# Kernel optimization log

Measured on AMD Instinct MI355X. Metric: run time of the kernel, lower is better.

## Reference

```python
import jax, jax.numpy as jnp
import numpy as np

B, T, L, F = 32, 512, 16, 128   # utterances, max frames, frame-spec width, specgram_height
H = 128                          # hidden_size1 == hidden_size2
C = 61                           # TIMIT phoneme count


def _p(key, shape, scale):
    return jax.random.normal(key, shape, jnp.float32) * scale


def setup_inputs() -> dict:
    key = jax.random.key(0)
    ks = jax.random.split(key, 32)
    s = 1.0 / np.sqrt(H)
    inp = {}
    inp["x"] = jax.random.normal(ks[0], (B, T, L, F), jnp.float32)
    inp["lengths"] = jax.random.randint(ks[1], (B,), T // 2, T + 1, jnp.int32)
    i = 2
    # rnn1: tanh-RNN, 2 layers, bidirectional (layer0 in=F, layer1 in=2H); dir axis 0
    for name, din in (("r1l0", F), ("r1l1", 2 * H)):
        inp[name + "_Wih"] = _p(ks[i], (2, H, din), s); i += 1
        inp[name + "_Whh"] = _p(ks[i], (2, H, H), s); i += 1
        inp[name + "_bih"] = _p(ks[i], (2, H), s); i += 1
        inp[name + "_bhh"] = _p(ks[i], (2, H), s); i += 1
    # rnn2: GRU, 2 layers, bidirectional (in=2H for both layers); gates packed r,z,n
    for name in ("g0", "g1"):
        inp[name + "_Wih"] = _p(ks[i], (2, 3 * H, 2 * H), s); i += 1
        inp[name + "_Whh"] = _p(ks[i], (2, 3 * H, H), s); i += 1
        inp[name + "_bih"] = _p(ks[i], (2, 3 * H), s); i += 1
        inp[name + "_bhh"] = _p(ks[i], (2, 3 * H), s); i += 1
    inp["fc_W"] = _p(ks[i], (C, 2 * H), s); i += 1
    inp["fc_b"] = _p(ks[i], (C,), s)
    return inp


def _rnn_bidir(x, Wih, Whh, bih, bhh):
    # x: (N, S, din) -> (N, S, 2H); PyTorch nn.RNN(tanh), bidirectional
    outs = []
    for d in range(2):
        xw = jnp.einsum('bli,hi->blh', x, Wih[d]) + bih[d]
        W, b = Whh[d], bhh[d]
        def step(h, xt):
            h = jnp.tanh(xt + h @ W.T + b)
            return h, h
        h0 = jnp.zeros((x.shape[0], W.shape[0]), x.dtype)
        _, ys = jax.lax.scan(step, h0, jnp.swapaxes(xw, 0, 1), reverse=(d == 1))
        outs.append(jnp.swapaxes(ys, 0, 1))
    return jnp.concatenate(outs, -1)


def _gru_bidir(x, Wih, Whh, bih, bhh):
    # x: (N, S, din) -> (N, S, 2H); PyTorch nn.GRU, bidirectional
    outs = []
    for d in range(2):
        xw = jnp.einsum('bli,hi->blh', x, Wih[d]) + bih[d]  # (N, S, 3H)
        W, b = Whh[d], bhh[d]
        def step(h, xt):
            g = h @ W.T + b
            xr, xz, xn = jnp.split(xt, 3, -1)
            gr, gz, gn = jnp.split(g, 3, -1)
            r = jax.nn.sigmoid(xr + gr)
            z = jax.nn.sigmoid(xz + gz)
            n = jnp.tanh(xn + r * gn)
            h = (1.0 - z) * n + z * h
            return h, h
        h0 = jnp.zeros((x.shape[0], W.shape[1]), x.dtype)
        _, ys = jax.lax.scan(step, h0, jnp.swapaxes(xw, 0, 1), reverse=(d == 1))
        outs.append(jnp.swapaxes(ys, 0, 1))
    return jnp.concatenate(outs, -1)


def reference(x, lengths,
              r1l0_Wih, r1l0_Whh, r1l0_bih, r1l0_bhh,
              r1l1_Wih, r1l1_Whh, r1l1_bih, r1l1_bhh,
              g0_Wih, g0_Whh, g0_bih, g0_bhh,
              g1_Wih, g1_Whh, g1_bih, g1_bhh,
              fc_W, fc_b):
    b, t, l, f = x.shape
    # per-sample rnn1 loop == one batched pass over all B*T frames (eval mode: no dropout)
    o = _rnn_bidir(x.reshape(b * t, l, f), r1l0_Wih, r1l0_Whh, r1l0_bih, r1l0_bhh)
    o = _rnn_bidir(o, r1l1_Wih, r1l1_Whh, r1l1_bih, r1l1_bhh)
    o = o[:, -1, :].reshape(b, t, 2 * H)       # last inner timestep per frame
    o = _gru_bidir(o, g0_Wih, g0_Whh, g0_bih, g0_bhh)
    o = _gru_bidir(o, g1_Wih, g1_Whh, g1_bih, g1_bhh)
    logits = o @ fc_W.T + fc_b                  # (B, T, C)
    mask = jnp.arange(t)[None, :] < lengths[:, None]
    # ragged scatter: concat first lengths[i] timesteps of each sample
    return logits.reshape(b * t, -1)[mask.reshape(-1)]
```

## Files before the change

### kernel.cpp

```cpp
#include <hip/hip_runtime.h>
#include <hip/hip_bf16.h>

#define B_ 32
#define T_ 512
#define L_ 16
#define F_ 128
#define H_ 128
#define C_ 61
#define NF_ (B_*T_)
#define CH_ 4096

typedef unsigned int u32;
typedef unsigned short u16;
typedef __attribute__((ext_vector_type(8))) short s16x8;
typedef __attribute__((ext_vector_type(4))) float f32x4;

__device__ __forceinline__ float bflo(u32 v){ return __uint_as_float(v << 16); }
__device__ __forceinline__ float bfhi(u32 v){ return __uint_as_float(v & 0xffff0000u); }
__device__ __forceinline__ u16 f2bf(float f){
  u32 u = __float_as_uint(f);
  u += 0x7fffu + ((u >> 16) & 1u);
  return (u16)(u >> 16);
}
__device__ __forceinline__ u32 pack2(float a, float b){
  return (u32)f2bf(a) | ((u32)f2bf(b) << 16);
}
__device__ __forceinline__ float fast_tanh(float x){
  float e = __expf(2.f*x);
  return 1.f - 2.f*__builtin_amdgcn_rcpf(e + 1.f);
}
__device__ __forceinline__ float fast_sigmoid(float x){
  return __builtin_amdgcn_rcpf(1.f + __expf(-x));
}
__device__ __forceinline__ f32x4 mfma16(s16x8 a, s16x8 b, f32x4 c){
  return __builtin_amdgcn_mfma_f32_16x16x32_bf16(a, b, c, 0, 0, 0);
}
__device__ __forceinline__ s16x8 packfrag(const float* p){
  const float4 a = *(const float4*)p;
  const float4 b = *(const float4*)(p+4);
  union { s16x8 v; u32 w[4]; } f;
  f.w[0]=pack2(a.x,a.y); f.w[1]=pack2(a.z,a.w);
  f.w[2]=pack2(b.x,b.y); f.w[3]=pack2(b.z,b.w);
  return f.v;
}

__global__ __launch_bounds__(256) void l0_mfma(
    const float* __restrict__ x,
    const float* __restrict__ Wih,
    const float* __restrict__ Whh,
    const float* __restrict__ bih,
    const float* __restrict__ bhh,
    u16* __restrict__ out)
{
  __shared__ __align__(16) u16 Hb[2][32][136];
  __shared__ __align__(16) u16 Xb[2][32][136];
  const int t = threadIdx.x;
  const int lane = t & 63, wv = t >> 6;
  const int l15 = lane & 15, kg = lane >> 4;
  const int dir = blockIdx.y;
  const int f0 = blockIdx.x * 32;
  s16x8 wih[2][4], whh[2][4];
  {
    const float* Wid = Wih + dir*16384;
    const float* Whd = Whh + dir*16384;
    #pragma unroll
    for (int nt = 0; nt < 2; nt++){
      const int u = wv*32 + nt*16 + l15;
      #pragma unroll
      for (int kc = 0; kc < 4; kc++){
        const int k = kc*32 + kg*8;
        wih[nt][kc] = packfrag(&Wid[u*128 + k]);
        whh[nt][kc] = packfrag(&Whd[u*128 + k]);
      }
    }
  }
  float bv[2];
  bv[0] = bih[dir*128 + wv*32 + l15]      + bhh[dir*128 + wv*32 + l15];
  bv[1] = bih[dir*128 + wv*32 + 16 + l15] + bhh[dir*128 + wv*32 + 16 + l15];
  const int sr = t >> 3, sc = (t & 7) * 16;
  {
    *(uint4*)&Hb[0][sr][sc]   = make_uint4(0,0,0,0);
    *(uint4*)&Hb[0][sr][sc+8] = make_uint4(0,0,0,0);
    const int s0 = dir ? 15 : 0;
    const float4* xp = (const float4*)&x[(size_t)(f0+sr)*2048 + s0*128 + sc];
    const float4 v0 = xp[0], v1 = xp[1], v2 = xp[2], v3 = xp[3];
    *(uint4*)&Xb[0][sr][sc]   = make_uint4(pack2(v0.x,v0.y),pack2(v0.z,v0.w),
                                           pack2(v1.x,v1.y),pack2(v1.z,v1.w));
    *(uint4*)&Xb[0][sr][sc+8] = make_uint4(pack2(v2.x,v2.y),pack2(v2.z,v2.w),
                                           pack2(v3.x,v3.y),pack2(v3.z,v3.w));
  }
  __syncthreads();
  int cur = 0;
  for (int st = 0; st < 16; st++){
    const int s = dir ? (15-st) : st;
    float4 p0,p1,p2,p3;
    if (st < 15){
      const int sn = dir ? (14-st) : (st+1);
      const float4* xp = (const float4*)&x[(size_t)(f0+sr)*2048 + sn*128 + sc];
      p0 = xp[0]; p1 = xp[1]; p2 = xp[2]; p3 = xp[3];
    }
    f32x4 acc00 = {0.f,0.f,0.f,0.f}, acc01 = acc00, acc10 = acc00, acc11 = acc00;
    #pragma unroll
    for (int kc = 0; kc < 4; kc++){
      const int ko = kc*32 + kg*8;
      const s16x8 ax0 = *(const s16x8*)&Xb[cur][l15][ko];
      const s16x8 ax1 = *(const s16x8*)&Xb[cur][16+l15][ko];
      const s16x8 ah0 = *(const s16x8*)&Hb[cur][l15][ko];
      const s16x8 ah1 = *(const s16x8*)&Hb[cur][16+l15][ko];
      acc00 = mfma16(ax0, wih[0][kc], acc00);
      acc01 = mfma16(ax0, wih[1][kc], acc01);
      acc10 = mfma16(ax1, wih[0][kc], acc10);
      acc11 = mfma16(ax1, wih[1][kc], acc11);
      acc00 = mfma16(ah0, whh[0][kc], acc00);
      acc01 = mfma16(ah0, whh[1][kc], acc01);
      acc10 = mfma16(ah1, whh[0][kc], acc10);
      acc11 = mfma16(ah1, whh[1][kc], acc11);
    }
    const int u0 = wv*32 + l15, u1 = wv*32 + 16 + l15;
    u16* op = out + (size_t)f0*4096 + s*256 + dir*128;
    #pragma unroll
    for (int r = 0; r < 4; r++){
      const int m0r = kg*4 + r, m1r = 16 + kg*4 + r;
      u16 h00 = f2bf(fast_tanh(acc00[r] + bv[0]));
      u16 h01 = f2bf(fast_tanh(acc01[r] + bv[1]));
      u16 h10 = f2bf(fast_tanh(acc10[r] + bv[0]));
      u16 h11 = f2bf(fast_tanh(acc11[r] + bv[1]));
      Hb[cur^1][m0r][u0] = h00;
      Hb[cur^1][m0r][u1] = h01;
      Hb[cur^1][m1r][u0] = h10;
      Hb[cur^1][m1r][u1] = h11;
      op[(size_t)m0r*4096 + u0] = h00;
      op[(size_t)m0r*4096 + u1] = h01;
      op[(size_t)m1r*4096 + u0] = h10;
      op[(size_t)m1r*4096 + u1] = h11;
    }
    if (st < 15){
      *(uint4*)&Xb[cur^1][sr][sc]   = make_uint4(pack2(p0.x,p0.y),pack2(p0.z,p0.w),
                                                 pack2(p1.x,p1.y),pack2(p1.z,p1.w));
      *(uint4*)&Xb[cur^1][sr][sc+8] = make_uint4(pack2(p2.x,p2.y),pack2(p2.z,p2.w),
                                                 pack2(p3.x,p3.y),pack2(p3.z,p3.w));
    }
    __syncthreads();
    cur ^= 1;
  }
}

__global__ __launch_bounds__(256) void l1f_mfma(
    const u16* __restrict__ U,
    const float* __restrict__ Wih,
    const float* __restrict__ Whh,
    const float* __restrict__ bih,
    const float* __restrict__ bhh,
    u16* __restrict__ out)
{
  __shared__ __align__(16) u16 Hb[2][16][136];
  __shared__ __align__(16) u16 Xb[2][16][264];
  const int t = threadIdx.x;
  const int lane = t & 63, wv = t >> 6;
  const int l15 = lane & 15, kg = lane >> 4;
  const int f0 = blockIdx.x * 16;
  s16x8 wih[2][8], whh[2][4];
  {
    #pragma unroll
    for (int nt = 0; nt < 2; nt++){
      const int u = wv*32 + nt*16 + l15;
      #pragma unroll
      for (int kc = 0; kc < 8; kc++)
        wih[nt][kc] = packfrag(&Wih[u*256 + kc*32 + kg*8]);
      #pragma unroll
      for (int kc = 0; kc < 4; kc++)
        whh[nt][kc] = packfrag(&Whh[u*128 + kc*32 + kg*8]);
    }
  }
  float bv[2];
  bv[0] = bih[wv*32 + l15]      + bhh[wv*32 + l15];
  bv[1] = bih[wv*32 + 16 + l15] + bhh[wv*32 + 16 + l15];
  const int sr = t >> 4, scu = (t & 15) * 16;
  for (int idx = t; idx < 272; idx += 256)
    ((uint4*)&Hb[0][0][0])[idx] = make_uint4(0,0,0,0);
  {
    const uint4* up = (const uint4*)&U[(size_t)(f0+sr)*4096 + scu];
    uint4 c0 = up[0], c1 = up[1];
    *(uint4*)&Xb[0][sr][scu]   = c0;
    *(uint4*)&Xb[0][sr][scu+8] = c1;
  }
  __syncthreads();
  int cur = 0;
  for (int st = 0; st < 16; st++){
    uint4 c0,c1;
    if (st < 15){
      const uint4* up = (const uint4*)&U[(size_t)(f0+sr)*4096 + (st+1)*256 + scu];
      c0 = up[0]; c1 = up[1];
    }
    f32x4 acc0 = {0.f,0.f,0.f,0.f}, acc1 = acc0;
    #pragma unroll
    for (int kc = 0; kc < 8; kc++){
      const s16x8 ax = *(const s16x8*)&Xb[cur][l15][kc*32 + kg*8];
      acc0 = mfma16(ax, wih[0][kc], acc0);
      acc1 = mfma16(ax, wih[1][kc], acc1);
    }
    #pragma unroll
    for (int kc = 0; kc < 4; kc++){
      const s16x8 ah = *(const s16x8*)&Hb[cur][l15][kc*32 + kg*8];
      acc0 = mfma16(ah, whh[0][kc], acc0);
      acc1 = mfma16(ah, whh[1][kc], acc1);
    }
    const int u0 = wv*32 + l15, u1 = wv*32 + 16 + l15;
    #pragma unroll
    for (int r = 0; r < 4; r++){
      const int m = kg*4 + r;
      const u16 h0 = f2bf(fast_tanh(acc0[r] + bv[0]));
      const u16 h1 = f2bf(fast_tanh(acc1[r] + bv[1]));
      Hb[cur^1][m][u0] = h0;
      Hb[cur^1][m][u1] = h1;
      if (st == 15){
        out[(size_t)(f0+m)*256 + u0] = h0;
        out[(size_t)(f0+m)*256 + u1] = h1;
      }
    }
    if (st < 15){
      *(uint4*)&Xb[cur^1][sr][scu]   = c0;
      *(uint4*)&Xb[cur^1][sr][scu+8] = c1;
    }
    __syncthreads();
    cur ^= 1;
  }
}

__global__ __launch_bounds__(256) void mfma_gemm(
    const u16* __restrict__ A, int lda,
    const u16* __restrict__ Wb, int K,
    const float* __restrict__ bias,
    float* __restrict__ Cf, u16* __restrict__ Cb, int ldc, int act)
{
  const int t = threadIdx.x;
  const int lane = t & 63, wv = t >> 6;
  const int l15 = lane & 15, kg = lane >> 4;
  const int n0 = blockIdx.x * 32;
  const int m0 = blockIdx.y * 64 + wv*16;
  const u16* Ap = A + (size_t)(m0 + l15)*lda + kg*8;
  const u16* W0 = Wb + (size_t)(n0 + l15)*K + kg*8;
  const u16* W1 = Wb + (size_t)(n0 + 16 + l15)*K + kg*8;
  f32x4 acc0 = {0.f,0.f,0.f,0.f}, acc1 = acc0;
  #pragma unroll 4
  for (int kc = 0; kc < K/32; kc++){
    const s16x8 a  = *(const s16x8*)(Ap + kc*32);
    const s16x8 b0 = *(const s16x8*)(W0 + kc*32);
    const s16x8 b1 = *(const s16x8*)(W1 + kc*32);
    acc0 = mfma16(a, b0, acc0);
    acc1 = mfma16(a, b1, acc1);
  }
  const int col0 = n0 + l15, col1 = n0 + 16 + l15;
  const float bv0 = bias[col0], bv1 = bias[col1];
  #pragma unroll
  for (int r = 0; r < 4; r++){
    const int row = m0 + kg*4 + r;
    float v0 = acc0[r] + bv0, v1 = acc1[r] + bv1;
    if (act){ v0 = fast_tanh(v0); v1 = fast_tanh(v1); }
    if (Cf){
      Cf[(size_t)row*ldc + col0] = v0;
      Cf[(size_t)row*ldc + col1] = v1;
    } else {
      Cb[(size_t)row*ldc + col0] = f2bf(v0);
      Cb[(size_t)row*ldc + col1] = f2bf(v1);
    }
  }
}

__global__ __launch_bounds__(256) void gemm_xw(
    const u16* __restrict__ A, int lda,
    const u16* __restrict__ Wb, int K,
    const float* __restrict__ bias,
    float* __restrict__ xwT)
{
  const int t = threadIdx.x;
  const int lane = t & 63, wv = t >> 6;
  const int l15 = lane & 15, kg = lane >> 4;
  const int n0 = blockIdx.x * 32;
  const int m0 = blockIdx.y * 64 + wv*16;
  const u16* Ap = A + (size_t)(m0 + l15)*lda + kg*8;
  const u16* W0 = Wb + (size_t)(n0 + l15)*K + kg*8;
  const u16* W1 = Wb + (size_t)(n0 + 16 + l15)*K + kg*8;
  f32x4 acc0 = {0.f,0.f,0.f,0.f}, acc1 = acc0;
  #pragma unroll 4
  for (int kc = 0; kc < K/32; kc++){
    const s16x8 a  = *(const s16x8*)(Ap + kc*32);
    const s16x8 b0 = *(const s16x8*)(W0 + kc*32);
    const s16x8 b1 = *(const s16x8*)(W1 + kc*32);
    acc0 = mfma16(a, b0, acc0);
    acc1 = mfma16(a, b1, acc1);
  }
  const int col0 = n0 + l15, col1 = n0 + 16 + l15;
  const float bv0 = bias[col0], bv1 = bias[col1];
  const int row0 = m0 + kg*4;
  const int b   = row0 >> 9;
  const int tt0 = row0 & 511;
  const int half = b >> 4, kg2 = (b & 15) >> 2, r2 = b & 3;
  const int d0 = col0 >= 384, d1 = col1 >= 384;
  const int cc0 = col0 - d0*384, cc1 = col1 - d1*384;
  const size_t i0 = (((((size_t)d0*512 + tt0)*2 + half)*8 + (cc0>>7? 0:0) + ((cc0&127)>>4))*4 + kg2)*192
                    + (size_t)(cc0&15)*12 + (cc0>>7)*4 + r2;
  const size_t i1 = (((((size_t)d1*512 + tt0)*2 + half)*8 + ((cc1&127)>>4))*4 + kg2)*192
                    + (size_t)(cc1&15)*12 + (cc1>>7)*4 + r2;
  #pragma unroll
  for (int r = 0; r < 4; r++){
    xwT[i0 + (size_t)r*12288] = acc0[r] + bv0;
    xwT[i1 + (size_t)r*12288] = acc1[r] + bv1;
  }
}

__global__ __launch_bounds__(256) void prep_kernel(
    const float* __restrict__ g0W, const float* __restrict__ g1W,
    const float* __restrict__ r1Wih,
    const float* __restrict__ r1bih, const float* __restrict__ r1bhh,
    u16* __restrict__ g0o, u16* __restrict__ g1o, u16* __restrict__ r1o,
    float* __restrict__ bo)
{
  const int i = blockIdx.x*256 + threadIdx.x;
  if (i < 196608){ g0o[i] = f2bf(g0W[i]); g1o[i] = f2bf(g1W[i]); }
  if (i < 32768)   r1o[i] = f2bf(r1Wih[32768 + i]);
  if (i < 128)     bo[i]  = r1bih[128+i] + r1bhh[128+i];
}

__global__ __launch_bounds__(512) void gru_mfma(
    const float* __restrict__ xwT,
    const float* __restrict__ Whh,
    const float* __restrict__ bhh,
    u16* __restrict__ hout)
{
  __shared__ __align__(16) u16 h_lds[2][16][136];
  const int t = threadIdx.x;
  const int lane = t & 63, wv = t >> 6;
  const int l15 = lane & 15, kg = lane >> 4;
  const int dir = blockIdx.x & 1, half = blockIdx.x >> 1;
  const int b0 = half*16;
  const int us = wv*16;
  s16x8 wb[3][4];
  {
    const float* Wd = Whh + (size_t)dir*49152;
    #pragma unroll
    for (int g = 0; g < 3; g++)
      #pragma unroll
      for (int kc = 0; kc < 4; kc++)
        wb[g][kc] = packfrag(&Wd[(size_t)(g*128 + us + l15)*128 + kc*32 + kg*8]);
  }
  const float bh0 = bhh[dir*384 + us + l15];
  const float bh1 = bhh[dir*384 + 128 + us + l15];
  const float bh2 = bhh[dir*384 + 256 + us + l15];
  if (t < 272) ((uint4*)&h_lds[0][0][0])[t] = make_uint4(0,0,0,0);
  float hreg[4] = {0.f,0.f,0.f,0.f};
  const long tstep = dir ? -49152 : 49152;
  const char* xb = (const char*)xwT
      + ((size_t)dir*512 + (dir ? 511 : 0))*49152
      + (size_t)((((half*8 + wv)*4 + kg)*16 + l15)*12)*4;
  f32x4 px0[3], px1[3];
  px0[0] = *(const f32x4*)(xb); px0[1] = *(const f32x4*)(xb+16); px0[2] = *(const f32x4*)(xb+32);
  xb += tstep;
  px1[0] = *(const f32x4*)(xb); px1[1] = *(const f32x4*)(xb+16); px1[2] = *(const f32x4*)(xb+32);
  xb += tstep;
  const int hstep = dir ? -256 : 256;
  int hoff[4];
  #pragma unroll
  for (int r = 0; r < 4; r++)
    hoff[r] = ((b0 + kg*4 + r)*512 + (dir ? 511 : 0))*256 + dir*128 + us + l15;
  __syncthreads();
  int cur = 0;

#define GSTEP(PX)                                                           \
  {                                                                         \
    const s16x8 af0 = *(const s16x8*)&h_lds[cur][l15][kg*8];                \
    const s16x8 af1 = *(const s16x8*)&h_lds[cur][l15][32+kg*8];             \
    const s16x8 af2 = *(const s16x8*)&h_lds[cur][l15][64+kg*8];             \
    const s16x8 af3 = *(const s16x8*)&h_lds[cur][l15][96+kg*8];             \
    f32x4 a0 = {0.f,0.f,0.f,0.f}, a1 = a0, a2 = a0;                         \
    a0 = mfma16(af0, wb[0][0], a0);                                         \
    a1 = mfma16(af0, wb[1][0], a1);                                         \
    a2 = mfma16(af0, wb[2][0], a2);                                         \
    a0 = mfma16(af1, wb[0][1], a0);                                         \
    a1 = mfma16(af1, wb[1][1], a1);                                         \
    a2 = mfma16(af1, wb[2][1], a2);                                         \
    a0 = mfma16(af2, wb[0][2], a0);                                         \
    a1 = mfma16(af2, wb[1][2], a1);                                         \
    a2 = mfma16(af2, wb[2][2], a2);                                         \
    a0 = mfma16(af3, wb[0][3], a0);                                         \
    a1 = mfma16(af3, wb[1][3], a1);                                         \
    a2 = mfma16(af3, wb[2][3], a2);                                         \
    const f32x4 n0 = *(const f32x4*)(xb);                                   \
    const f32x4 n1 = *(const f32x4*)(xb+16);                                \
    const f32x4 n2 = *(const f32x4*)(xb+32);                                \
    xb += tstep;                                                            \
    _Pragma("unroll")                                                       \
    for (int r = 0; r < 4; r++){                                            \
      const float rr = fast_sigmoid(PX[0][r] + a0[r] + bh0);                \
      const float zz = fast_sigmoid(PX[1][r] + a1[r] + bh1);                \
      const float nn = fast_tanh(PX[2][r] + rr*(a2[r] + bh2));              \
      const float hn = fmaf(zz, hreg[r]-nn, nn);                            \
      hreg[r] = hn;                                                         \
      const u16 hb = f2bf(hn);                                              \
      h_lds[cur^1][kg*4+r][us+l15] = hb;                                    \
      hout[hoff[r]] = hb;                                                   \
      hoff[r] += hstep;                                                     \
    }                                                                       \
    PX[0] = n0; PX[1] = n1; PX[2] = n2;                                     \
    __syncthreads();                                                        \
    cur ^= 1;                                                               \
  }

  for (int ti = 0; ti < 512; ti += 2){
    GSTEP(px0);
    GSTEP(px1);
  }
#undef GSTEP
}

__global__ void prefix_kernel(const int* __restrict__ lengths, int* __restrict__ pre){
  if (threadIdx.x == 0 && blockIdx.x == 0){
    int run = 0;
    for (int b = 0; b < 32; b++){ pre[b] = run; run += lengths[b]; }
  }
}

__global__ __launch_bounds__(256) void fc_kernel(
    const u16* __restrict__ A,
    const float* __restrict__ W,
    const float* __restrict__ bias,
    const int* __restrict__ lengths,
    const int* __restrict__ pre,
    float* __restrict__ out)
{
  __shared__ __align__(16) float4 Wl[64][61];
  __shared__ __align__(16) float  Al[64][256];
  const int t = threadIdx.x;
  const int row0 = blockIdx.x * 64;
  for (int idx = t; idx < 61*64; idx += 256){
    int c = idx >> 6, k4 = idx & 63;
    Wl[k4][c] = *(const float4*)&W[(size_t)c*256 + k4*4];
  }
  {
    const u32* A32 = (const u32*)(A + (size_t)row0*256);
    for (int idx = t; idx < 8192; idx += 256){
      u32 v = A32[idx];
      int r = idx >> 7, kp = idx & 127;
      Al[r][2*kp]   = bflo(v);
      Al[r][2*kp+1] = bfhi(v);
    }
  }
  __syncthreads();
  const int c = t & 63;
  const int rbase = t >> 6;
  if (c < 61){
    const float bv = bias[c];
    for (int rr = rbase; rr < 64; rr += 4){
      float s0=0,s1=0,s2=0,s3=0;
      const float4* Ap = (const float4*)&Al[rr][0];
      #pragma unroll
      for (int k4 = 0; k4 < 64; k4++){
        const float4 w = Wl[k4][c];
        const float4 a = Ap[k4];
        s0 = fmaf(w.x, a.x, s0);
        s1 = fmaf(w.y, a.y, s1);
        s2 = fmaf(w.z, a.z, s2);
        s3 = fmaf(w.w, a.w, s3);
      }
      const int n = row0 + rr;
      const int b = n >> 9, tt = n & 511;
      if (tt < lengths[b])
        out[(size_t)(pre[b] + tt)*61 + c] = bv + s0+s1+s2+s3;
    }
  }
}

extern "C" void kernel_launch(void* const* d_in, const int* in_sizes, int n_in,
                              void* d_out, int out_size, void* d_ws, size_t ws_size,
                              hipStream_t stream)
{
  const float* x     = (const float*)d_in[0];
  const int*   lens  = (const int*)d_in[1];
  const float* r0Wih = (const float*)d_in[2];
  const float* r0Whh = (const float*)d_in[3];
  const float* r0bih = (const float*)d_in[4];
  const float* r0bhh = (const float*)d_in[5];
  const float* r1Wih = (const float*)d_in[6];
  const float* r1Whh = (const float*)d_in[7];
  const float* r1bih = (const float*)d_in[8];
  const float* r1bhh = (const float*)d_in[9];
  const float* g0Wih = (const float*)d_in[10];
  const float* g0Whh = (const float*)d_in[11];
  const float* g0bih = (const float*)d_in[12];
  const float* g0bhh = (const float*)d_in[13];
  const float* g1Wih = (const float*)d_in[14];
  const float* g1Whh = (const float*)d_in[15];
  const float* g1bih = (const float*)d_in[16];
  const float* g1bhh = (const float*)d_in[17];
  const float* fcW   = (const float*)d_in[18];
  const float* fcb   = (const float*)d_in[19];
  float* out = (float*)d_out;

  char* ws = (char*)d_ws;
  u16*   l0buf = (u16*)(ws);
  float* xwbuf = (float*)(ws);
  u16*   g0out = (u16*)(ws + 50331648);
  u16*   g0Wb  = (u16*)(ws + 58720256);
  u16*   g1Wb  = (u16*)(ws + 58720256 + 393216);
  u16*   r1Wb  = (u16*)(ws + 58720256 + 786432);
  float* biasb = (float*)(ws + 58720256 + 851968);
  u16*   g1out = (u16*)(ws + 58720256);
  u16*   rnn1  = (u16*)(ws + 67108864);
  int*   pre   = (int*)(ws + 75497472);

  prep_kernel<<<768, 256, 0, stream>>>(g0Wih, g1Wih, r1Wih, r1bih, r1bhh,
                                       g0Wb, g1Wb, r1Wb, biasb);
  for (int c = 0; c < NF_/CH_; c++){
    l0_mfma<<<dim3(CH_/32, 2), 256, 0, stream>>>(
        x + (size_t)c*CH_*2048, r0Wih, r0Whh, r0bih, r0bhh, l0buf);
    l1f_mfma<<<dim3(CH_/16), 256, 0, stream>>>(
        l0buf, r1Wih, r1Whh, r1bih, r1bhh, rnn1 + (size_t)c*CH_*256);
    mfma_gemm<<<dim3(128/32, CH_/64), 256, 0, stream>>>(
        l0buf + 15*256, 4096, r1Wb, 256, biasb,
        (float*)nullptr, rnn1 + (size_t)c*CH_*256 + 128, 256, 1);
  }
  gemm_xw<<<dim3(768/32, NF_/64), 256, 0, stream>>>(
      rnn1, 256, g0Wb, 256, g0bih, xwbuf);
  gru_mfma<<<4, 512, 0, stream>>>(xwbuf, g0Whh, g0bhh, g0out);
  gemm_xw<<<dim3(768/32, NF_/64), 256, 0, stream>>>(
      g0out, 256, g1Wb, 256, g1bih, xwbuf);
  gru_mfma<<<4, 512, 0, stream>>>(xwbuf, g1Whh, g1bhh, g1out);
  prefix_kernel<<<1, 64, 0, stream>>>(lens, pre);
  fc_kernel<<<NF_/64, 256, 0, stream>>>(g1out, fcW, fcb, lens, pre, out);
}
```

Measured before the change: 1.163 ms.

## Restructure GRU recurrence to 4 waves with transposed MFMA and folded r/z biases

The GRU recurrent kernel now runs 256 threads (4 waves) per block instead of 512, with each wave owning 32 hidden units across two 16-wide tiles. The MFMA operands are swapped so that each lane holds 4 consecutive hidden units, which lets h be written to LDS and global memory as packed uint2 stores. The xw precompute now folds the recurrent r and z biases into its output and writes a matching new layout. The intent is to cut per-step barrier cost and scalar store traffic on the serial critical path. In exchange each wave carries twice the weight registers and does twice the gate math per step, and the out-of-bounds prefetch on the final steps is dropped.

```diff
diff --git a/kernel.cpp b/kernel.cpp
--- a/kernel.cpp
+++ b/kernel.cpp
@@ -270,7 +270,7 @@
 __global__ __launch_bounds__(256) void gemm_xw(
     const u16* __restrict__ A, int lda,
     const u16* __restrict__ Wb, int K,
-    const float* __restrict__ bias,
+    const float* __restrict__ bih, const float* __restrict__ bhhp,
     float* __restrict__ xwT)
 {
   const int t = threadIdx.x;
@@ -291,17 +291,31 @@
     acc1 = mfma16(a, b1, acc1);
   }
   const int col0 = n0 + l15, col1 = n0 + 16 + l15;
-  const float bv0 = bias[col0], bv1 = bias[col1];
   const int row0 = m0 + kg*4;
-  const int b   = row0 >> 9;
-  const int tt0 = row0 & 511;
-  const int half = b >> 4, kg2 = (b & 15) >> 2, r2 = b & 3;
-  const int d0 = col0 >= 384, d1 = col1 >= 384;
-  const int cc0 = col0 - d0*384, cc1 = col1 - d1*384;
-  const size_t i0 = (((((size_t)d0*512 + tt0)*2 + half)*8 + (cc0>>7? 0:0) + ((cc0&127)>>4))*4 + kg2)*192
-                    + (size_t)(cc0&15)*12 + (cc0>>7)*4 + r2;
-  const size_t i1 = (((((size_t)d1*512 + tt0)*2 + half)*8 + ((cc1&127)>>4))*4 + kg2)*192
-                    + (size_t)(cc1&15)*12 + (cc1>>7)*4 + r2;
+  const int b = row0 >> 9, tt0 = row0 & 511;
+  const int half = b >> 4, bl = b & 15;
+  float bv0 = bih[col0], bv1 = bih[col1];
+  {
+    const int c0 = col0 >= 384 ? col0-384 : col0;
+    const int c1 = col1 >= 384 ? col1-384 : col1;
+    if ((c0 >> 7) < 2) bv0 += bhhp[col0];
+    if ((c1 >> 7) < 2) bv1 += bhhp[col1];
+  }
+  size_t i0, i1;
+  {
+    const int d0 = col0 >= 384 ? 1 : 0;
+    const int c  = col0 - d0*384;
+    const int g = c >> 7, cu = c & 127;
+    i0 = (((((size_t)d0*512 + tt0)*2 + half)*4 + (cu>>5))*4 + ((cu>>2)&3))*384
+         + (size_t)bl*24 + ((cu>>4)&1)*12 + g*4 + (cu&3);
+  }
+  {
+    const int d1 = col1 >= 384 ? 1 : 0;
+    const int c  = col1 - d1*384;
+    const int g = c >> 7, cu = c & 127;
+    i1 = (((((size_t)d1*512 + tt0)*2 + half)*4 + (cu>>5))*4 + ((cu>>2)&3))*384
+         + (size_t)bl*24 + ((cu>>4)&1)*12 + g*4 + (cu&3);
+  }
   #pragma unroll
   for (int r = 0; r < 4; r++){
     xwT[i0 + (size_t)r*12288] = acc0[r] + bv0;
@@ -322,7 +336,7 @@
   if (i < 128)     bo[i]  = r1bih[128+i] + r1bhh[128+i];
 }
 
-__global__ __launch_bounds__(512) void gru_mfma(
+__global__ __launch_bounds__(256, 1) void gru_mfma(
     const float* __restrict__ xwT,
     const float* __restrict__ Whh,
     const float* __restrict__ bhh,
@@ -333,83 +347,95 @@
   const int lane = t & 63, wv = t >> 6;
   const int l15 = lane & 15, kg = lane >> 4;
   const int dir = blockIdx.x & 1, half = blockIdx.x >> 1;
-  const int b0 = half*16;
-  const int us = wv*16;
-  s16x8 wb[3][4];
+  s16x8 wa[2][3][4];
   {
     const float* Wd = Whh + (size_t)dir*49152;
     #pragma unroll
-    for (int g = 0; g < 3; g++)
+    for (int t2 = 0; t2 < 2; t2++)
       #pragma unroll
-      for (int kc = 0; kc < 4; kc++)
-        wb[g][kc] = packfrag(&Wd[(size_t)(g*128 + us + l15)*128 + kc*32 + kg*8]);
-  }
-  const float bh0 = bhh[dir*384 + us + l15];
-  const float bh1 = bhh[dir*384 + 128 + us + l15];
-  const float bh2 = bhh[dir*384 + 256 + us + l15];
-  if (t < 272) ((uint4*)&h_lds[0][0][0])[t] = make_uint4(0,0,0,0);
-  float hreg[4] = {0.f,0.f,0.f,0.f};
-  const long tstep = dir ? -49152 : 49152;
+      for (int g = 0; g < 3; g++)
+        #pragma unroll
+        for (int kc = 0; kc < 4; kc++)
+          wa[t2][g][kc] = packfrag(&Wd[(size_t)(g*128 + wv*32 + t2*16 + l15)*128
+                                       + kc*32 + kg*8]);
+  }
+  f32x4 bhn[2];
+  bhn[0] = *(const f32x4*)&bhh[dir*384 + 256 + wv*32 + kg*4];
+  bhn[1] = *(const f32x4*)&bhh[dir*384 + 256 + wv*32 + 16 + kg*4];
+  {
+    const uint4 z = make_uint4(0,0,0,0);
+    ((uint4*)h_lds)[t] = z;
+    if (t < 16) ((uint4*)h_lds)[256 + t] = z;
+  }
+  f32x4 hreg[2] = {{0.f,0.f,0.f,0.f},{0.f,0.f,0.f,0.f}};
+  const long tstep = dir ? -49152L : 49152L;
   const char* xb = (const char*)xwT
       + ((size_t)dir*512 + (dir ? 511 : 0))*49152
-      + (size_t)((((half*8 + wv)*4 + kg)*16 + l15)*12)*4;
-  f32x4 px0[3], px1[3];
-  px0[0] = *(const f32x4*)(xb); px0[1] = *(const f32x4*)(xb+16); px0[2] = *(const f32x4*)(xb+32);
+      + (size_t)((((half*4 + wv)*4 + kg)*16 + l15)*24)*4;
+  f32x4 pa[6], pb[6];
+  #pragma unroll
+  for (int j = 0; j < 6; j++) pa[j] = *(const f32x4*)(xb + j*16);
   xb += tstep;
-  px1[0] = *(const f32x4*)(xb); px1[1] = *(const f32x4*)(xb+16); px1[2] = *(const f32x4*)(xb+32);
+  #pragma unroll
+  for (int j = 0; j < 6; j++) pb[j] = *(const f32x4*)(xb + j*16);
   xb += tstep;
   const int hstep = dir ? -256 : 256;
-  int hoff[4];
-  #pragma unroll
-  for (int r = 0; r < 4; r++)
-    hoff[r] = ((b0 + kg*4 + r)*512 + (dir ? 511 : 0))*256 + dir*128 + us + l15;
+  int hoff = ((half*16 + l15)*512 + (dir ? 511 : 0))*256 + dir*128 + wv*32 + kg*4;
   __syncthreads();
   int cur = 0;
 
-#define GSTEP(PX)                                                           \
+#define GSTEP(PX, DOLOAD)                                                   \
   {                                                                         \
-    const s16x8 af0 = *(const s16x8*)&h_lds[cur][l15][kg*8];                \
-    const s16x8 af1 = *(const s16x8*)&h_lds[cur][l15][32+kg*8];             \
-    const s16x8 af2 = *(const s16x8*)&h_lds[cur][l15][64+kg*8];             \
-    const s16x8 af3 = *(const s16x8*)&h_lds[cur][l15][96+kg*8];             \
-    f32x4 a0 = {0.f,0.f,0.f,0.f}, a1 = a0, a2 = a0;                         \
-    a0 = mfma16(af0, wb[0][0], a0);                                         \
-    a1 = mfma16(af0, wb[1][0], a1);                                         \
-    a2 = mfma16(af0, wb[2][0], a2);                                         \
-    a0 = mfma16(af1, wb[0][1], a0);                                         \
-    a1 = mfma16(af1, wb[1][1], a1);                                         \
-    a2 = mfma16(af1, wb[2][1], a2);                                         \
-    a0 = mfma16(af2, wb[0][2], a0);                                         \
-    a1 = mfma16(af2, wb[1][2], a1);                                         \
-    a2 = mfma16(af2, wb[2][2], a2);                                         \
-    a0 = mfma16(af3, wb[0][3], a0);                                         \
-    a1 = mfma16(af3, wb[1][3], a1);                                         \
-    a2 = mfma16(af3, wb[2][3], a2);                                         \
-    const f32x4 n0 = *(const f32x4*)(xb);                                   \
-    const f32x4 n1 = *(const f32x4*)(xb+16);                                \
-    const f32x4 n2 = *(const f32x4*)(xb+32);                                \
-    xb += tstep;                                                            \
+    f32x4 acc[2][3] = {{{0.f,0.f,0.f,0.f},{0.f,0.f,0.f,0.f},               \
+                        {0.f,0.f,0.f,0.f}},                                 \
+                       {{0.f,0.f,0.f,0.f},{0.f,0.f,0.f,0.f},               \
+                        {0.f,0.f,0.f,0.f}}};                                \
     _Pragma("unroll")                                                       \
-    for (int r = 0; r < 4; r++){                                            \
-      const float rr = fast_sigmoid(PX[0][r] + a0[r] + bh0);                \
-      const float zz = fast_sigmoid(PX[1][r] + a1[r] + bh1);                \
-      const float nn = fast_tanh(PX[2][r] + rr*(a2[r] + bh2));              \
-      const float hn = fmaf(zz, hreg[r]-nn, nn);                            \
-      hreg[r] = hn;                                                         \
-      const u16 hb = f2bf(hn);                                              \
-      h_lds[cur^1][kg*4+r][us+l15] = hb;                                    \
-      hout[hoff[r]] = hb;                                                   \
-      hoff[r] += hstep;                                                     \
+    for (int kc = 0; kc < 4; kc++){                                         \
+      const s16x8 hf = *(const s16x8*)&h_lds[cur][l15][kc*32 + kg*8];       \
+      _Pragma("unroll")                                                     \
+      for (int t2 = 0; t2 < 2; t2++)                                        \
+        _Pragma("unroll")                                                   \
+        for (int g = 0; g < 3; g++)                                         \
+          acc[t2][g] = mfma16(wa[t2][g][kc], hf, acc[t2][g]);               \
     }                                                                       \
-    PX[0] = n0; PX[1] = n1; PX[2] = n2;                                     \
+    f32x4 nx0,nx1,nx2,nx3,nx4,nx5;                                          \
+    if (DOLOAD){                                                            \
+      nx0 = *(const f32x4*)(xb);     nx1 = *(const f32x4*)(xb+16);          \
+      nx2 = *(const f32x4*)(xb+32);  nx3 = *(const f32x4*)(xb+48);          \
+      nx4 = *(const f32x4*)(xb+64);  nx5 = *(const f32x4*)(xb+80);          \
+      xb += tstep;                                                          \
+    }                                                                       \
+    _Pragma("unroll")                                                       \
+    for (int t2 = 0; t2 < 2; t2++){                                         \
+      float hn[4];                                                          \
+      _Pragma("unroll")                                                     \
+      for (int r = 0; r < 4; r++){                                          \
+        const float rr = fast_sigmoid(PX[t2*3+0][r] + acc[t2][0][r]);       \
+        const float zz = fast_sigmoid(PX[t2*3+1][r] + acc[t2][1][r]);       \
+        const float nn = fast_tanh(PX[t2*3+2][r]                            \
+                                   + rr*(acc[t2][2][r] + bhn[t2][r]));      \
+        hn[r] = fmaf(zz, hreg[t2][r] - nn, nn);                             \
+        hreg[t2][r] = hn[r];                                                \
+      }                                                                     \
+      const uint2 hp = make_uint2(pack2(hn[0],hn[1]), pack2(hn[2],hn[3]));  \
+      *(uint2*)&h_lds[cur^1][l15][wv*32 + t2*16 + kg*4] = hp;               \
+      *(uint2*)&hout[hoff + t2*16] = hp;                                    \
+    }                                                                       \
+    hoff += hstep;                                                          \
+    if (DOLOAD){                                                            \
+      PX[0]=nx0; PX[1]=nx1; PX[2]=nx2; PX[3]=nx3; PX[4]=nx4; PX[5]=nx5;     \
+    }                                                                       \
     __syncthreads();                                                        \
     cur ^= 1;                                                               \
   }
 
-  for (int ti = 0; ti < 512; ti += 2){
-    GSTEP(px0);
-    GSTEP(px1);
-  }
+  for (int ti = 0; ti < 510; ti += 2){
+    GSTEP(pa, 1);
+    GSTEP(pb, 1);
+  }
+  GSTEP(pa, 0);
+  GSTEP(pb, 0);
 #undef GSTEP
 }
 
@@ -520,11 +546,11 @@
         (float*)nullptr, rnn1 + (size_t)c*CH_*256 + 128, 256, 1);
   }
   gemm_xw<<<dim3(768/32, NF_/64), 256, 0, stream>>>(
-      rnn1, 256, g0Wb, 256, g0bih, xwbuf);
-  gru_mfma<<<4, 512, 0, stream>>>(xwbuf, g0Whh, g0bhh, g0out);
+      rnn1, 256, g0Wb, 256, g0bih, g0bhh, xwbuf);
+  gru_mfma<<<4, 256, 0, stream>>>(xwbuf, g0Whh, g0bhh, g0out);
   gemm_xw<<<dim3(768/32, NF_/64), 256, 0, stream>>>(
-      g0out, 256, g1Wb, 256, g1bih, xwbuf);
-  gru_mfma<<<4, 512, 0, stream>>>(xwbuf, g1Whh, g1bhh, g1out);
+      g0out, 256, g1Wb, 256, g1bih, g1bhh, xwbuf);
+  gru_mfma<<<4, 256, 0, stream>>>(xwbuf, g1Whh, g1bhh, g1out);
   prefix_kernel<<<1, 64, 0, stream>>>(lens, pre);
   fc_kernel<<<NF_/64, 256, 0, stream>>>(g1out, fcW, fcb, lens, pre, out);
 }
```

Result: slower. 1.191 ms (+2.4%).
